# Optimization experiments

Hardware: AMD Instinct MI355X
Metric: run time of the kernel (lower is better)

## Reference

```python
import jax, jax.numpy as jnp
import numpy as np

B, S, D, H = 2, 2048, 512, 8
E = D // H  # per-head depth = 64


def setup_inputs() -> dict:
    key = jax.random.key(0)
    ks = jax.random.split(key, 10)
    x = jax.random.normal(ks[0], (B, S, D), dtype=jnp.float32)
    # binary mask: 1 = masked position (added as -1e9)
    attention_mask = jax.random.randint(ks[1], (B, S, S), 0, 2, dtype=jnp.int32)
    # per-head Dense weights stacked: [H, D, E] (Keras Dense: y = x @ W + b)
    sc = 1.0 / np.sqrt(D)
    Wq = jax.random.normal(ks[2], (H, D, E), dtype=jnp.float32) * sc
    Wk = jax.random.normal(ks[3], (H, D, E), dtype=jnp.float32) * sc
    Wv = jax.random.normal(ks[4], (H, D, E), dtype=jnp.float32) * sc
    bq = jnp.zeros((H, E), dtype=jnp.float32)
    bk = jnp.zeros((H, E), dtype=jnp.float32)
    bv = jnp.zeros((H, E), dtype=jnp.float32)
    Wo = jax.random.normal(ks[5], (D, D), dtype=jnp.float32) * sc
    bo = jnp.zeros((D,), dtype=jnp.float32)
    return {"x": x, "attention_mask": attention_mask, "Wq": Wq, "bq": bq,
            "Wk": Wk, "bk": bk, "Wv": Wv, "bv": bv, "Wo": Wo, "bo": bo}


def reference(x, attention_mask, Wq, bq, Wk, bk, Wv, bv, Wo, bo):
    # Per-head Dense projections, vectorized over heads: [B,H,S,E]
    q = jnp.einsum('bsd,hde->bhse', x, Wq) + bq[None, :, None, :]
    k = jnp.einsum('bsd,hde->bhse', x, Wk) + bk[None, :, None, :]
    v = jnp.einsum('bsd,hde->bhse', x, Wv) + bv[None, :, None, :]
    # scaled dot-product attention
    scores = jnp.einsum('bhse,bhte->bhst', q, k) / jnp.sqrt(jnp.float32(E))
    scores = scores + (-1e9) * attention_mask.astype(jnp.float32)[:, None, :, :]
    weights = jax.nn.softmax(scores, axis=-1)
    o = jnp.einsum('bhst,bhte->bhse', weights, v)
    # concat heads (head i -> columns [i*E:(i+1)*E]) then output Dense
    o = o.transpose(0, 2, 1, 3).reshape(B, S, D)
    return o @ Wo + bo
```

## Files before the change

### kernel.cpp

```cpp
#include <hip/hip_runtime.h>
#include <hip/hip_bf16.h>

typedef unsigned short u16;
typedef unsigned int u32;
typedef unsigned long long u64;
typedef short s16x8 __attribute__((ext_vector_type(8)));
typedef float f32x4 __attribute__((ext_vector_type(4)));
typedef float f32x16 __attribute__((ext_vector_type(16)));
typedef int i32x4 __attribute__((ext_vector_type(4)));

static __device__ __forceinline__ u16 f2b(float f) {
    union { float f; unsigned u; } x; x.f = f;
    unsigned r = x.u + 0x7fffu + ((x.u >> 16) & 1u);
    return (u16)(r >> 16);
}

static __device__ __forceinline__ u32 pkbf2(float a, float b) {
    union { __hip_bfloat162 h; u32 u; } c;
    c.h = __float22bfloat162_rn(make_float2(a, b));
    return c.u;
}

static __device__ __forceinline__ f32x16 zero16() {
    f32x16 z;
#pragma unroll
    for (int i = 0; i < 16; i++) z[i] = 0.f;
    return z;
}

static __device__ __forceinline__ s16x8 mk8(u32 a, u32 b, u32 c, u32 d) {
    union { u32 u[4]; s16x8 v; } x;
    x.u[0] = a; x.u[1] = b; x.u[2] = c; x.u[3] = d;
    return x.v;
}

static __device__ __forceinline__ u32 sx32(u32 v) {
    return (u32)__shfl_xor((int)v, 32, 64);
}

static __device__ __forceinline__ void gll16(const u16* g, u16* l) {
    __builtin_amdgcn_global_load_lds(
        (const __attribute__((address_space(1))) u32*)g,
        (__attribute__((address_space(3))) u32*)l, 16, 0, 0);
}


__global__ __launch_bounds__(256)
void k_pack_all(const float* __restrict__ x, const int* __restrict__ mask,
                const float* __restrict__ Wq, const float* __restrict__ Wk,
                const float* __restrict__ Wv, const float* __restrict__ Wo,
                const float* __restrict__ bq, const float* __restrict__ bk,
                const float* __restrict__ bv, const float* __restrict__ bo,
                u16* __restrict__ xb, u16* __restrict__ WT, u16* __restrict__ WoT,
                float* __restrict__ bias, u32* __restrict__ mb) {
    int idx = blockIdx.x * 256 + threadIdx.x;
    if (idx < 524288) {
        int i = idx * 4;
        float4 v = *(const float4*)(x + i);
        ushort4 o;
        o.x = f2b(v.x); o.y = f2b(v.y); o.z = f2b(v.z); o.w = f2b(v.w);
        *(ushort4*)(xb + i) = o;
    } else if (idx < 1310720) {
        int t = idx - 524288;
        int z = t >> 18, r = t & 262143;
        const float* W = (z == 0) ? Wq : (z == 1) ? Wk : Wv;
        int n = r >> 9, d = r & 511;
        WT[t] = f2b(W[((n >> 6) * 512 + d) * 64 + (n & 63)]);
    } else if (idx < 1572864) {
        int r = idx - 1310720;
        int n = r >> 9, d = r & 511;
        WoT[r] = f2b(Wo[d * 512 + n]);
    } else if (idx < 1574912) {
        int i = idx - 1572864;
        float v;
        if (i < 512) v = bq[i];
        else if (i < 1024) v = bk[i - 512];
        else if (i < 1536) v = bv[i - 1024];
        else v = bo[i - 1536];
        bias[i] = v;
    } else {
        int i2 = idx - 1574912;
        const int* p = mask + (size_t)i2 * 32;
        unsigned wv2 = 0;
#pragma unroll
        for (int j = 0; j < 32; j += 4) {
            int4 v = *(const int4*)(p + j);
            wv2 |= ((unsigned)(v.x & 1) << j) | ((unsigned)(v.y & 1) << (j + 1)) |
                   ((unsigned)(v.z & 1) << (j + 2)) | ((unsigned)(v.w & 1) << (j + 3));
        }
        mb[i2] = wv2;
    }
}


template<int MF, bool F32OUT>
__global__ __launch_bounds__(256)
void k_gemm(const u16* __restrict__ A, const u16* __restrict__ BTbase,
            const float* __restrict__ biasBase,
            u16* __restrict__ Cb, u16* __restrict__ Vt, float* __restrict__ Cf) {
    const int BM = MF * 32;
    const int nblk = blockIdx.x, mblk = blockIdx.y, z = blockIdx.z;
    const u16* BT = BTbase + (size_t)z * 262144;
    const float* bias = biasBase + z * 512;
    __shared__ __align__(16) u16 As[MF * 32 * 64];
    __shared__ __align__(16) u16 Bs[128 * 64];
    const int tid = threadIdx.x, lane = tid & 63, wv = tid >> 6;
    const int lr = lane & 15, lg = lane >> 4;
    const int wr = (wv >> 1) * (MF * 16), wc = (wv & 1) * 64;
    const u16* Ag = A + (size_t)(mblk * BM) * 512;
    const u16* Bg = BT + (size_t)(nblk * 128) * 512;

    f32x4 acc[MF][4];
#pragma unroll
    for (int i = 0; i < MF; i++)
#pragma unroll
        for (int j = 0; j < 4; j++) acc[i][j] = (f32x4){0.f, 0.f, 0.f, 0.f};

    for (int kt = 0; kt < 8; kt++) {
        __syncthreads();
#pragma unroll
        for (int i = 0; i < MF; i++) {
            int f = i * 256 + tid, r = f >> 3, c = f & 7;
            *(i32x4*)&As[r * 64 + ((c * 8) ^ ((r & 7) << 3))] =
                *(const i32x4*)(Ag + (size_t)r * 512 + kt * 64 + c * 8);
        }
#pragma unroll
        for (int i = 0; i < 4; i++) {
            int f = i * 256 + tid, r = f >> 3, c = f & 7;
            *(i32x4*)&Bs[r * 64 + ((c * 8) ^ ((r & 7) << 3))] =
                *(const i32x4*)(Bg + (size_t)r * 512 + kt * 64 + c * 8);
        }
        __syncthreads();
#pragma unroll
        for (int ks = 0; ks < 2; ks++) {
            s16x8 af[MF], bf[4];
#pragma unroll
            for (int mf = 0; mf < MF; mf++) {
                int r = wr + mf * 16 + lr;
                af[mf] = *(const s16x8*)&As[r * 64 + ((ks * 32 + lg * 8) ^ ((r & 7) << 3))];
            }
#pragma unroll
            for (int nf = 0; nf < 4; nf++) {
                int r = wc + nf * 16 + lr;
                bf[nf] = *(const s16x8*)&Bs[r * 64 + ((ks * 32 + lg * 8) ^ ((r & 7) << 3))];
            }
#pragma unroll
            for (int mf = 0; mf < MF; mf++)
#pragma unroll
                for (int nf = 0; nf < 4; nf++)
                    acc[mf][nf] = __builtin_amdgcn_mfma_f32_16x16x32_bf16(
                        af[mf], bf[nf], acc[mf][nf], 0, 0, 0);
        }
    }
    const float qsc = (!F32OUT && z == 0) ? 0.18033688011112042f : 1.0f;
#pragma unroll
    for (int nf = 0; nf < 4; nf++) {
        int col = nblk * 128 + wc + nf * 16 + lr;
        float bval = bias[col];
#pragma unroll
        for (int mf = 0; mf < MF; mf++) {
            int row0 = mblk * BM + wr + mf * 16 + lg * 4;
            if (F32OUT) {
#pragma unroll
                for (int r = 0; r < 4; r++)
                    Cf[(size_t)(row0 + r) * 512 + col] = acc[mf][nf][r] + bval;
            } else if (z == 2) {
                ushort4 o;
                o.x = f2b(acc[mf][nf][0] + bval);
                o.y = f2b(acc[mf][nf][1] + bval);
                o.z = f2b(acc[mf][nf][2] + bval);
                o.w = f2b(acc[mf][nf][3] + bval);
                *(ushort4*)(Vt + (size_t)(row0 >> 11) * 1048576 +
                            (size_t)col * 2048 + (row0 & 2047)) = o;
            } else {
#pragma unroll
                for (int r = 0; r < 4; r++)
                    Cb[(size_t)z * 2097152 + (size_t)(row0 + r) * 512 + col] =
                        f2b((acc[mf][nf][r] + bval) * qsc);
            }
        }
    }
}


__global__ __launch_bounds__(512, 4)
void k_attn(const u16* __restrict__ qkv, const u16* __restrict__ vt,
            const u32* __restrict__ mb, u16* __restrict__ oc) {
    const int qt = blockIdx.x, h = blockIdx.y, b = blockIdx.z;
    const u16* Qb = qkv + (size_t)b * 1048576 + h * 64;
    const u16* Kb = Qb + 2097152;
    const u16* VtH = vt + (size_t)b * 1048576 + (size_t)h * 131072;

    __shared__ __align__(16) u16 SMEM[32768];
    __shared__ float Lbuf[8][32];

    const int tid = threadIdx.x;
    const int lane = tid & 63, w = tid >> 6;
    const int hi = lane >> 5, l31 = lane & 31;
    const int qg = w & 1, kvq = w >> 1;
    const int qrow = qt * 64 + qg * 32 + l31;

    const int lr8 = lane >> 3, lc8 = (lane & 7) ^ lr8;
    const int vr16 = lane >> 2, vc4 = (lane & 3) ^ ((lane >> 3) & 3);
    const int kvbase0 = kvq * 512;
    const int qoff = kvq * 4096;

    s16x8 qf[4];
#pragma unroll
    for (int ks = 0; ks < 4; ks++)
        qf[ks] = *(const s16x8*)(Qb + (size_t)qrow * 512 + ks * 16 + hi * 8);

#pragma unroll
    for (int i = 0; i < 2; i++) {
        gll16(Kb + (size_t)(kvbase0 + qg * 16 + i * 8 + lr8) * 512 + lc8 * 8,
              &SMEM[qoff + (qg * 16 + i * 8) * 64]);
        gll16(VtH + (size_t)(qg * 32 + i * 16 + vr16) * 2048 + kvbase0 + vc4 * 8,
              &SMEM[qoff + 2048 + qg * 1024 + i * 512]);
    }
    const int mbase = (b * 2048 + qrow) * 64 + kvq * 16;
    u32 mreg = mb[mbase];
    __syncthreads();

    f32x16 accO0 = zero16(), accO1 = zero16();
    f32x4 lvec = (f32x4){0.f, 0.f, 0.f, 0.f};
    const int kswz = (l31 & 7) << 3;
    const int vkey = (l31 >> 1) & 3;

    for (int t = 0; t < 16; t++) {
        const int bo = (t & 1) << 14;
        u32 mnx = 0;
        if (t < 15) {
            const int bn = bo ^ 16384;
            const int kvb = kvbase0 + (t + 1) * 32;
#pragma unroll
            for (int i = 0; i < 2; i++) {
                gll16(Kb + (size_t)(kvb + qg * 16 + i * 8 + lr8) * 512 + lc8 * 8,
                      &SMEM[bn + qoff + (qg * 16 + i * 8) * 64]);
                gll16(VtH + (size_t)(qg * 32 + i * 16 + vr16) * 2048 + kvb + vc4 * 8,
                      &SMEM[bn + qoff + 2048 + qg * 1024 + i * 512]);
            }
            mnx = mb[mbase + t + 1];
        }
        const u16* Kq = &SMEM[bo + qoff];
        const u16* Vq = &SMEM[bo + qoff + 2048];

        f32x16 sa = zero16();
        __builtin_amdgcn_s_setprio(1);
#pragma unroll
        for (int ks = 0; ks < 4; ks++) {
            const int cb = ks * 16 + hi * 8;
            s16x8 kf = *(const s16x8*)&Kq[l31 * 64 + (cb ^ kswz)];
            sa = __builtin_amdgcn_mfma_f32_32x32x16_bf16(kf, qf[ks], sa, 0, 0, 0);
        }
        __builtin_amdgcn_s_setprio(0);

        const u32 mw = mreg >> (hi * 4);
        u32 pk[8];
#pragma unroll
        for (int g = 0; g < 8; g++) {
            const int r0 = 2 * g, r1 = 2 * g + 1;
            const int p0 = (r0 & 3) + 8 * (r0 >> 2);
            const int p1 = (r1 & 3) + 8 * (r1 >> 2);
            float a = ((mw >> p0) & 1u) ? 0.f : __builtin_amdgcn_exp2f(sa[r0]);
            float b2 = ((mw >> p1) & 1u) ? 0.f : __builtin_amdgcn_exp2f(sa[r1]);
            lvec[r0 & 3] += a;
            lvec[r1 & 3] += b2;
            pk[g] = pkbf2(a, b2);
        }

        s16x8 pa[2];
        {
            u32 x0 = sx32(pk[0]), x1 = sx32(pk[1]), x2 = sx32(pk[2]), x3 = sx32(pk[3]);
            u32 x4 = sx32(pk[4]), x5 = sx32(pk[5]), x6 = sx32(pk[6]), x7 = sx32(pk[7]);
            pa[0] = mk8(hi ? x2 : pk[0], hi ? x3 : pk[1],
                        hi ? pk[2] : x0, hi ? pk[3] : x1);
            pa[1] = mk8(hi ? x6 : pk[4], hi ? x7 : pk[5],
                        hi ? pk[6] : x4, hi ? pk[7] : x5);
        }

        __builtin_amdgcn_s_setprio(1);
#pragma unroll
        for (int ksg = 0; ksg < 2; ksg++) {
            const int off = ((ksg * 2 + hi) ^ vkey) << 3;
            s16x8 bv0 = *(const s16x8*)&Vq[l31 * 32 + off];
            s16x8 bv1 = *(const s16x8*)&Vq[(32 + l31) * 32 + off];
            accO0 = __builtin_amdgcn_mfma_f32_32x32x16_bf16(pa[ksg], bv0, accO0, 0, 0, 0);
            accO1 = __builtin_amdgcn_mfma_f32_32x32x16_bf16(pa[ksg], bv1, accO1, 0, 0, 0);
        }
        __builtin_amdgcn_s_setprio(0);

        __syncthreads();
        mreg = mnx;
    }

    float Ls = (lvec[0] + lvec[1]) + (lvec[2] + lvec[3]);
    Ls += __shfl_xor(Ls, 32, 64);

    float* Obuf = (float*)SMEM;
    const int lx = (lane & 7) * 4;
    const int obase = w * 2048 + lane * 32;
#pragma unroll
    for (int g = 0; g < 4; g++) {
        *(f32x4*)&Obuf[obase + ((4 * g) ^ lx)] =
            (f32x4){accO0[4 * g], accO0[4 * g + 1], accO0[4 * g + 2], accO0[4 * g + 3]};
        *(f32x4*)&Obuf[obase + ((16 + 4 * g) ^ lx)] =
            (f32x4){accO1[4 * g], accO1[4 * g + 1], accO1[4 * g + 2], accO1[4 * g + 3]};
    }
    if (lane < 32) Lbuf[w][lane] = Ls;
    __syncthreads();

    const int qg2 = w & 1, rq = w >> 1;
    f32x4 v0[4], v1[4];
#pragma unroll
    for (int j = 0; j < 4; j++) {
        const int wp = qg2 + 2 * j;
        v0[j] = *(const f32x4*)&Obuf[wp * 2048 + lane * 32 + ((rq * 4) ^ lx)];
        v1[j] = *(const f32x4*)&Obuf[wp * 2048 + lane * 32 + ((16 + rq * 4) ^ lx)];
    }
#pragma unroll
    for (int k = 0; k < 4; k++) {
        const int q_k = k + 8 * rq + 4 * hi;
        float D = Lbuf[qg2][q_k] + Lbuf[qg2 + 2][q_k] +
                  Lbuf[qg2 + 4][q_k] + Lbuf[qg2 + 6][q_k];
        float inv = 1.0f / D;
        float o0 = (v0[0][k] + v0[1][k] + v0[2][k] + v0[3][k]) * inv;
        float o1 = (v1[0][k] + v1[1][k] + v1[2][k] + v1[3][k]) * inv;
        const size_t orow = ((size_t)b * 2048 + qt * 64 + qg2 * 32 + q_k) * 512 + h * 64;
        oc[orow + l31]      = f2b(o0);
        oc[orow + 32 + l31] = f2b(o1);
    }
}


extern "C" void kernel_launch(void* const* d_in, const int* in_sizes, int n_in,
                              void* d_out, int out_size, void* d_ws, size_t ws_size,
                              hipStream_t stream) {
    const float* x    = (const float*)d_in[0];
    const int*   mask = (const int*)d_in[1];
    const float* Wq   = (const float*)d_in[2];
    const float* bq   = (const float*)d_in[3];
    const float* Wk   = (const float*)d_in[4];
    const float* bk   = (const float*)d_in[5];
    const float* Wv   = (const float*)d_in[6];
    const float* bv   = (const float*)d_in[7];
    const float* Wo   = (const float*)d_in[8];
    const float* bo   = (const float*)d_in[9];

    u16* xb     = (u16*)d_ws;
    u16* WT     = xb + 2097152;
    u16* WoT    = WT + 786432;
    u16* qkv    = WoT + 262144;
    u16* vtp    = qkv + 4194304;
    u16* oc     = qkv + 6291456;
    float* bias = (float*)(oc + 2097152);
    u32* mbits  = (u32*)(bias + 2048);

    k_pack_all<<<7176, 256, 0, stream>>>(x, mask, Wq, Wk, Wv, Wo, bq, bk, bv, bo,
                                         xb, WT, WoT, bias, mbits);
    k_gemm<2, false><<<dim3(4, 64, 3), 256, 0, stream>>>(xb, WT, bias, qkv, vtp, nullptr);
    k_attn<<<dim3(32, 8, 2), 512, 0, stream>>>(qkv, vtp, mbits, oc);
    k_gemm<2, true><<<dim3(4, 64, 1), 256, 0, stream>>>(oc, WoT, bias + 1536,
                                                        nullptr, nullptr, (float*)d_out);
}
```

Measured before the change: 78.80 us.

## Replace mask bits with bf16 AND masks and compute row sums via MFMA

```diff
diff --git a/kernel.cpp b/kernel.cpp
--- a/kernel.cpp
+++ b/kernel.cpp
@@ -52,7 +52,7 @@
                 const float* __restrict__ bq, const float* __restrict__ bk,
                 const float* __restrict__ bv, const float* __restrict__ bo,
                 u16* __restrict__ xb, u16* __restrict__ WT, u16* __restrict__ WoT,
-                float* __restrict__ bias, u32* __restrict__ mb) {
+                float* __restrict__ bias, u32* __restrict__ mand) {
     int idx = blockIdx.x * 256 + threadIdx.x;
     if (idx < 524288) {
         int i = idx * 4;
@@ -80,15 +80,18 @@
         bias[i] = v;
     } else {
         int i2 = idx - 1574912;
-        const int* p = mask + (size_t)i2 * 32;
-        unsigned wv2 = 0;
-#pragma unroll
-        for (int j = 0; j < 32; j += 4) {
-            int4 v = *(const int4*)(p + j);
-            wv2 |= ((unsigned)(v.x & 1) << j) | ((unsigned)(v.y & 1) << (j + 1)) |
-                   ((unsigned)(v.z & 1) << (j + 2)) | ((unsigned)(v.w & 1) << (j + 3));
-        }
-        mb[i2] = wv2;
+        const int4* p = (const int4*)(mask + (size_t)i2 * 32);
+        u32* op = mand + (size_t)i2 * 16;
+#pragma unroll
+        for (int k = 0; k < 4; k++) {
+            int4 v0 = p[2 * k], v1 = p[2 * k + 1];
+            uint4 o;
+            o.x = (v0.x ? 0u : 0xFFFFu) | (v0.y ? 0u : 0xFFFF0000u);
+            o.y = (v0.z ? 0u : 0xFFFFu) | (v0.w ? 0u : 0xFFFF0000u);
+            o.z = (v1.x ? 0u : 0xFFFFu) | (v1.y ? 0u : 0xFFFF0000u);
+            o.w = (v1.z ? 0u : 0xFFFFu) | (v1.w ? 0u : 0xFFFF0000u);
+            *(uint4*)(op + 4 * k) = o;
+        }
     }
 }
 
@@ -185,7 +188,7 @@
 
 __global__ __launch_bounds__(512, 4)
 void k_attn(const u16* __restrict__ qkv, const u16* __restrict__ vt,
-            const u32* __restrict__ mb, u16* __restrict__ oc) {
+            const u32* __restrict__ mand, u16* __restrict__ oc) {
     const int qt = blockIdx.x, h = blockIdx.y, b = blockIdx.z;
     const u16* Qb = qkv + (size_t)b * 1048576 + h * 64;
     const u16* Kb = Qb + 2097152;
@@ -210,36 +213,40 @@
     for (int ks = 0; ks < 4; ks++)
         qf[ks] = *(const s16x8*)(Qb + (size_t)qrow * 512 + ks * 16 + hi * 8);
 
-#pragma unroll
-    for (int i = 0; i < 2; i++) {
-        gll16(Kb + (size_t)(kvbase0 + qg * 16 + i * 8 + lr8) * 512 + lc8 * 8,
-              &SMEM[qoff + (qg * 16 + i * 8) * 64]);
-        gll16(VtH + (size_t)(qg * 32 + i * 16 + vr16) * 2048 + kvbase0 + vc4 * 8,
-              &SMEM[qoff + 2048 + qg * 1024 + i * 512]);
-    }
-    const int mbase = (b * 2048 + qrow) * 64 + kvq * 16;
-    u32 mreg = mb[mbase];
+    const u16* kptr = Kb + (size_t)(kvbase0 + qg * 16 + lr8) * 512 + lc8 * 8;
+    const u16* vptr = VtH + (size_t)(qg * 32 + vr16) * 2048 + kvbase0 + vc4 * 8;
+    const u32* mptr = mand + (size_t)(b * 2048 + qrow) * 1024 + kvq * 256 + 2 * hi;
+
+    gll16(kptr, &SMEM[qoff + (qg * 16) * 64]);
+    gll16(kptr + 4096, &SMEM[qoff + (qg * 16 + 8) * 64]);
+    gll16(vptr, &SMEM[qoff + 2048 + qg * 1024]);
+    gll16(vptr + 32768, &SMEM[qoff + 2048 + qg * 1024 + 512]);
+    uint2 mm0 = *(const uint2*)(mptr);
+    uint2 mm1 = *(const uint2*)(mptr + 4);
+    uint2 mm2 = *(const uint2*)(mptr + 8);
+    uint2 mm3 = *(const uint2*)(mptr + 12);
+    kptr += 16384; vptr += 32; mptr += 16;
     __syncthreads();
 
-    f32x16 accO0 = zero16(), accO1 = zero16();
-    f32x4 lvec = (f32x4){0.f, 0.f, 0.f, 0.f};
+    f32x16 accO0 = zero16(), accO1 = zero16(), lacc = zero16();
+    const s16x8 onesv = mk8(0x3F803F80u, 0x3F803F80u, 0x3F803F80u, 0x3F803F80u);
     const int kswz = (l31 & 7) << 3;
     const int vkey = (l31 >> 1) & 3;
 
     for (int t = 0; t < 16; t++) {
         const int bo = (t & 1) << 14;
-        u32 mnx = 0;
+        uint2 mn0, mn1, mn2, mn3;
         if (t < 15) {
             const int bn = bo ^ 16384;
-            const int kvb = kvbase0 + (t + 1) * 32;
-#pragma unroll
-            for (int i = 0; i < 2; i++) {
-                gll16(Kb + (size_t)(kvb + qg * 16 + i * 8 + lr8) * 512 + lc8 * 8,
-                      &SMEM[bn + qoff + (qg * 16 + i * 8) * 64]);
-                gll16(VtH + (size_t)(qg * 32 + i * 16 + vr16) * 2048 + kvb + vc4 * 8,
-                      &SMEM[bn + qoff + 2048 + qg * 1024 + i * 512]);
-            }
-            mnx = mb[mbase + t + 1];
+            gll16(kptr, &SMEM[bn + qoff + (qg * 16) * 64]);
+            gll16(kptr + 4096, &SMEM[bn + qoff + (qg * 16 + 8) * 64]);
+            gll16(vptr, &SMEM[bn + qoff + 2048 + qg * 1024]);
+            gll16(vptr + 32768, &SMEM[bn + qoff + 2048 + qg * 1024 + 512]);
+            mn0 = *(const uint2*)(mptr);
+            mn1 = *(const uint2*)(mptr + 4);
+            mn2 = *(const uint2*)(mptr + 8);
+            mn3 = *(const uint2*)(mptr + 12);
+            kptr += 16384; vptr += 32; mptr += 16;
         }
         const u16* Kq = &SMEM[bo + qoff];
         const u16* Vq = &SMEM[bo + qoff + 2048];
@@ -254,19 +261,17 @@
         }
         __builtin_amdgcn_s_setprio(0);
 
-        const u32 mw = mreg >> (hi * 4);
         u32 pk[8];
 #pragma unroll
         for (int g = 0; g < 8; g++) {
-            const int r0 = 2 * g, r1 = 2 * g + 1;
-            const int p0 = (r0 & 3) + 8 * (r0 >> 2);
-            const int p1 = (r1 & 3) + 8 * (r1 >> 2);
-            float a = ((mw >> p0) & 1u) ? 0.f : __builtin_amdgcn_exp2f(sa[r0]);
-            float b2 = ((mw >> p1) & 1u) ? 0.f : __builtin_amdgcn_exp2f(sa[r1]);
-            lvec[r0 & 3] += a;
-            lvec[r1 & 3] += b2;
+            float a = __builtin_amdgcn_exp2f(sa[2 * g]);
+            float b2 = __builtin_amdgcn_exp2f(sa[2 * g + 1]);
             pk[g] = pkbf2(a, b2);
         }
+        pk[0] &= mm0.x; pk[1] &= mm0.y;
+        pk[2] &= mm1.x; pk[3] &= mm1.y;
+        pk[4] &= mm2.x; pk[5] &= mm2.y;
+        pk[6] &= mm3.x; pk[7] &= mm3.y;
 
         s16x8 pa[2];
         {
@@ -287,18 +292,24 @@
             accO0 = __builtin_amdgcn_mfma_f32_32x32x16_bf16(pa[ksg], bv0, accO0, 0, 0, 0);
             accO1 = __builtin_amdgcn_mfma_f32_32x32x16_bf16(pa[ksg], bv1, accO1, 0, 0, 0);
         }
+        lacc = __builtin_amdgcn_mfma_f32_32x32x16_bf16(pa[0], onesv, lacc, 0, 0, 0);
+        lacc = __builtin_amdgcn_mfma_f32_32x32x16_bf16(pa[1], onesv, lacc, 0, 0, 0);
         __builtin_amdgcn_s_setprio(0);
 
         __syncthreads();
-        mreg = mnx;
-    }
-
-    float Ls = (lvec[0] + lvec[1]) + (lvec[2] + lvec[3]);
-    Ls += __shfl_xor(Ls, 32, 64);
+        if (t < 15) { mm0 = mn0; mm1 = mn1; mm2 = mn2; mm3 = mn3; }
+    }
+
+    if (l31 == 0) {
+#pragma unroll
+        for (int r = 0; r < 16; r++)
+            Lbuf[w][(r & 3) + 8 * (r >> 2) + 4 * hi] = lacc[r];
+    }
 
     float* Obuf = (float*)SMEM;
     const int lx = (lane & 7) * 4;
     const int obase = w * 2048 + lane * 32;
+    __syncthreads();
 #pragma unroll
     for (int g = 0; g < 4; g++) {
         *(f32x4*)&Obuf[obase + ((4 * g) ^ lx)] =
@@ -306,7 +317,6 @@
         *(f32x4*)&Obuf[obase + ((16 + 4 * g) ^ lx)] =
             (f32x4){accO1[4 * g], accO1[4 * g + 1], accO1[4 * g + 2], accO1[4 * g + 3]};
     }
-    if (lane < 32) Lbuf[w][lane] = Ls;
     __syncthreads();
 
     const int qg2 = w & 1, rq = w >> 1;
@@ -353,12 +363,12 @@
     u16* vtp    = qkv + 4194304;
     u16* oc     = qkv + 6291456;
     float* bias = (float*)(oc + 2097152);
-    u32* mbits  = (u32*)(bias + 2048);
+    u32* mand   = (u32*)(bias + 2048);
 
     k_pack_all<<<7176, 256, 0, stream>>>(x, mask, Wq, Wk, Wv, Wo, bq, bk, bv, bo,
-                                         xb, WT, WoT, bias, mbits);
+                                         xb, WT, WoT, bias, mand);
     k_gemm<2, false><<<dim3(4, 64, 3), 256, 0, stream>>>(xb, WT, bias, qkv, vtp, nullptr);
-    k_attn<<<dim3(32, 8, 2), 512, 0, stream>>>(qkv, vtp, mbits, oc);
+    k_attn<<<dim3(32, 8, 2), 512, 0, stream>>>(qkv, vtp, mand, oc);
     k_gemm<2, true><<<dim3(4, 64, 1), 256, 0, stream>>>(oc, WoT, bias + 1536,
                                                         nullptr, nullptr, (float*)d_out);
 }
```

After: 101.7 us. +29.0%, slower.

## Restructure attention to 4 waves each owning KV quarter for 64 query rows

Applied to the files above, without the earlier changes.

```diff
diff --git a/kernel.cpp b/kernel.cpp
--- a/kernel.cpp
+++ b/kernel.cpp
@@ -183,7 +183,7 @@
 }
 
 
-__global__ __launch_bounds__(512, 4)
+__global__ __launch_bounds__(256, 2)
 void k_attn(const u16* __restrict__ qkv, const u16* __restrict__ vt,
             const u32* __restrict__ mb, u16* __restrict__ oc) {
     const int qt = blockIdx.x, h = blockIdx.y, b = blockIdx.z;
@@ -192,90 +192,112 @@
     const u16* VtH = vt + (size_t)b * 1048576 + (size_t)h * 131072;
 
     __shared__ __align__(16) u16 SMEM[32768];
-    __shared__ float Lbuf[8][32];
+    __shared__ float Lbuf[4][64];
 
     const int tid = threadIdx.x;
     const int lane = tid & 63, w = tid >> 6;
     const int hi = lane >> 5, l31 = lane & 31;
-    const int qg = w & 1, kvq = w >> 1;
-    const int qrow = qt * 64 + qg * 32 + l31;
+    const int qrow = qt * 64 + l31;
+
+    s16x8 qfl[4], qfh[4];
+#pragma unroll
+    for (int ks = 0; ks < 4; ks++) {
+        qfl[ks] = *(const s16x8*)(Qb + (size_t)qrow * 512 + ks * 16 + hi * 8);
+        qfh[ks] = *(const s16x8*)(Qb + (size_t)(qrow + 32) * 512 + ks * 16 + hi * 8);
+    }
 
     const int lr8 = lane >> 3, lc8 = (lane & 7) ^ lr8;
     const int vr16 = lane >> 2, vc4 = (lane & 3) ^ ((lane >> 3) & 3);
-    const int kvbase0 = kvq * 512;
-    const int qoff = kvq * 4096;
-
-    s16x8 qf[4];
-#pragma unroll
-    for (int ks = 0; ks < 4; ks++)
-        qf[ks] = *(const s16x8*)(Qb + (size_t)qrow * 512 + ks * 16 + hi * 8);
-
-#pragma unroll
-    for (int i = 0; i < 2; i++) {
-        gll16(Kb + (size_t)(kvbase0 + qg * 16 + i * 8 + lr8) * 512 + lc8 * 8,
-              &SMEM[qoff + (qg * 16 + i * 8) * 64]);
-        gll16(VtH + (size_t)(qg * 32 + i * 16 + vr16) * 2048 + kvbase0 + vc4 * 8,
-              &SMEM[qoff + 2048 + qg * 1024 + i * 512]);
-    }
-    const int mbase = (b * 2048 + qrow) * 64 + kvq * 16;
-    u32 mreg = mb[mbase];
-    __syncthreads();
-
-    f32x16 accO0 = zero16(), accO1 = zero16();
-    f32x4 lvec = (f32x4){0.f, 0.f, 0.f, 0.f};
+    const int kv0 = w * 512;
+
+    const u16* kptr = Kb + (size_t)(kv0 + lr8) * 512 + lc8 * 8;
+    const u16* vptr = VtH + (size_t)vr16 * 2048 + kv0 + vc4 * 8;
+    const u32* mbl = mb + (size_t)(b * 2048 + qrow) * 64 + w * 16;
+    const u32* mbh = mbl + 2048;
+
+    u16* wbase = &SMEM[w * 8192];
+
+#pragma unroll
+    for (int i = 0; i < 4; i++) {
+        gll16(kptr + (size_t)(i * 8) * 512, wbase + i * 512);
+        gll16(vptr + (size_t)(i * 16) * 2048, wbase + 2048 + i * 512);
+    }
+    u32 ml = mbl[0], mh = mbh[0];
+
+    f32x16 aL0 = zero16(), aL1 = zero16(), aH0 = zero16(), aH1 = zero16();
+    f32x4 lvl = (f32x4){0.f, 0.f, 0.f, 0.f}, lvh = (f32x4){0.f, 0.f, 0.f, 0.f};
     const int kswz = (l31 & 7) << 3;
     const int vkey = (l31 >> 1) & 3;
 
     for (int t = 0; t < 16; t++) {
-        const int bo = (t & 1) << 14;
-        u32 mnx = 0;
+        const u16* Kq = wbase + (t & 1) * 4096;
+        const u16* Vq = Kq + 2048;
+        u32 mnl = 0, mnh = 0;
         if (t < 15) {
-            const int bn = bo ^ 16384;
-            const int kvb = kvbase0 + (t + 1) * 32;
-#pragma unroll
-            for (int i = 0; i < 2; i++) {
-                gll16(Kb + (size_t)(kvb + qg * 16 + i * 8 + lr8) * 512 + lc8 * 8,
-                      &SMEM[bn + qoff + (qg * 16 + i * 8) * 64]);
-                gll16(VtH + (size_t)(qg * 32 + i * 16 + vr16) * 2048 + kvb + vc4 * 8,
-                      &SMEM[bn + qoff + 2048 + qg * 1024 + i * 512]);
-            }
-            mnx = mb[mbase + t + 1];
-        }
-        const u16* Kq = &SMEM[bo + qoff];
-        const u16* Vq = &SMEM[bo + qoff + 2048];
-
-        f32x16 sa = zero16();
+            const u16* kp = kptr + (size_t)((t + 1) * 32) * 512;
+            const u16* vp = vptr + (t + 1) * 32;
+            u16* db = wbase + (((t + 1) & 1) << 12);
+#pragma unroll
+            for (int i = 0; i < 4; i++) {
+                gll16(kp + (size_t)(i * 8) * 512, db + i * 512);
+                gll16(vp + (size_t)(i * 16) * 2048, db + 2048 + i * 512);
+            }
+            mnl = mbl[t + 1];
+            mnh = mbh[t + 1];
+            asm volatile("s_waitcnt vmcnt(10)" ::: "memory");
+        } else {
+            asm volatile("s_waitcnt vmcnt(0)" ::: "memory");
+        }
+        __builtin_amdgcn_sched_barrier(0);
+
+        f32x16 sl = zero16(), sh = zero16();
         __builtin_amdgcn_s_setprio(1);
 #pragma unroll
         for (int ks = 0; ks < 4; ks++) {
-            const int cb = ks * 16 + hi * 8;
-            s16x8 kf = *(const s16x8*)&Kq[l31 * 64 + (cb ^ kswz)];
-            sa = __builtin_amdgcn_mfma_f32_32x32x16_bf16(kf, qf[ks], sa, 0, 0, 0);
+            s16x8 kf = *(const s16x8*)&Kq[l31 * 64 + ((ks * 16 + hi * 8) ^ kswz)];
+            sl = __builtin_amdgcn_mfma_f32_32x32x16_bf16(kf, qfl[ks], sl, 0, 0, 0);
+            sh = __builtin_amdgcn_mfma_f32_32x32x16_bf16(kf, qfh[ks], sh, 0, 0, 0);
         }
         __builtin_amdgcn_s_setprio(0);
 
-        const u32 mw = mreg >> (hi * 4);
-        u32 pk[8];
-#pragma unroll
-        for (int g = 0; g < 8; g++) {
-            const int r0 = 2 * g, r1 = 2 * g + 1;
-            const int p0 = (r0 & 3) + 8 * (r0 >> 2);
-            const int p1 = (r1 & 3) + 8 * (r1 >> 2);
-            float a = ((mw >> p0) & 1u) ? 0.f : __builtin_amdgcn_exp2f(sa[r0]);
-            float b2 = ((mw >> p1) & 1u) ? 0.f : __builtin_amdgcn_exp2f(sa[r1]);
-            lvec[r0 & 3] += a;
-            lvec[r1 & 3] += b2;
-            pk[g] = pkbf2(a, b2);
-        }
-
-        s16x8 pa[2];
+        s16x8 pal0, pal1, pah0, pah1;
         {
-            u32 x0 = sx32(pk[0]), x1 = sx32(pk[1]), x2 = sx32(pk[2]), x3 = sx32(pk[3]);
-            u32 x4 = sx32(pk[4]), x5 = sx32(pk[5]), x6 = sx32(pk[6]), x7 = sx32(pk[7]);
-            pa[0] = mk8(hi ? x2 : pk[0], hi ? x3 : pk[1],
-                        hi ? pk[2] : x0, hi ? pk[3] : x1);
-            pa[1] = mk8(hi ? x6 : pk[4], hi ? x7 : pk[5],
-                        hi ? pk[6] : x4, hi ? pk[7] : x5);
+            const u32 mw = ml >> (hi * 4);
+            u32 pk[8];
+#pragma unroll
+            for (int g = 0; g < 8; g++) {
+                const int p0 = ((2 * g) & 3) + 8 * (g >> 1);
+                float a = ((mw >> p0) & 1u) ? 0.f : __builtin_amdgcn_exp2f(sl[2 * g]);
+                float b2 = ((mw >> (p0 + 1)) & 1u) ? 0.f : __builtin_amdgcn_exp2f(sl[2 * g + 1]);
+                lvl[(2 * g) & 3] += a;
+                lvl[(2 * g + 1) & 3] += b2;
+                pk[g] = pkbf2(a, b2);
+            }
+            u32 xa = sx32(hi ? pk[0] : pk[2]);
+            u32 xb = sx32(hi ? pk[1] : pk[3]);
+            u32 xc = sx32(hi ? pk[4] : pk[6]);
+            u32 xd = sx32(hi ? pk[5] : pk[7]);
+            pal0 = hi ? mk8(xa, xb, pk[2], pk[3]) : mk8(pk[0], pk[1], xa, xb);
+            pal1 = hi ? mk8(xc, xd, pk[6], pk[7]) : mk8(pk[4], pk[5], xc, xd);
+        }
+        {
+            const u32 mw = mh >> (hi * 4);
+            u32 pk[8];
+#pragma unroll
+            for (int g = 0; g < 8; g++) {
+                const int p0 = ((2 * g) & 3) + 8 * (g >> 1);
+                float a = ((mw >> p0) & 1u) ? 0.f : __builtin_amdgcn_exp2f(sh[2 * g]);
+                float b2 = ((mw >> (p0 + 1)) & 1u) ? 0.f : __builtin_amdgcn_exp2f(sh[2 * g + 1]);
+                lvh[(2 * g) & 3] += a;
+                lvh[(2 * g + 1) & 3] += b2;
+                pk[g] = pkbf2(a, b2);
+            }
+            u32 xa = sx32(hi ? pk[0] : pk[2]);
+            u32 xb = sx32(hi ? pk[1] : pk[3]);
+            u32 xc = sx32(hi ? pk[4] : pk[6]);
+            u32 xd = sx32(hi ? pk[5] : pk[7]);
+            pah0 = hi ? mk8(xa, xb, pk[2], pk[3]) : mk8(pk[0], pk[1], xa, xb);
+            pah1 = hi ? mk8(xc, xd, pk[6], pk[7]) : mk8(pk[4], pk[5], xc, xd);
         }
 
         __builtin_amdgcn_s_setprio(1);
@@ -284,50 +306,59 @@
             const int off = ((ksg * 2 + hi) ^ vkey) << 3;
             s16x8 bv0 = *(const s16x8*)&Vq[l31 * 32 + off];
             s16x8 bv1 = *(const s16x8*)&Vq[(32 + l31) * 32 + off];
-            accO0 = __builtin_amdgcn_mfma_f32_32x32x16_bf16(pa[ksg], bv0, accO0, 0, 0, 0);
-            accO1 = __builtin_amdgcn_mfma_f32_32x32x16_bf16(pa[ksg], bv1, accO1, 0, 0, 0);
+            s16x8 pl = ksg ? pal1 : pal0;
+            s16x8 ph = ksg ? pah1 : pah0;
+            aL0 = __builtin_amdgcn_mfma_f32_32x32x16_bf16(pl, bv0, aL0, 0, 0, 0);
+            aL1 = __builtin_amdgcn_mfma_f32_32x32x16_bf16(pl, bv1, aL1, 0, 0, 0);
+            aH0 = __builtin_amdgcn_mfma_f32_32x32x16_bf16(ph, bv0, aH0, 0, 0, 0);
+            aH1 = __builtin_amdgcn_mfma_f32_32x32x16_bf16(ph, bv1, aH1, 0, 0, 0);
         }
         __builtin_amdgcn_s_setprio(0);
 
-        __syncthreads();
-        mreg = mnx;
-    }
-
-    float Ls = (lvec[0] + lvec[1]) + (lvec[2] + lvec[3]);
-    Ls += __shfl_xor(Ls, 32, 64);
+        ml = mnl; mh = mnh;
+    }
+
+    float Lsl = (lvl[0] + lvl[1]) + (lvl[2] + lvl[3]);
+    Lsl += __shfl_xor(Lsl, 32, 64);
+    float Lsh = (lvh[0] + lvh[1]) + (lvh[2] + lvh[3]);
+    Lsh += __shfl_xor(Lsh, 32, 64);
+    if (lane < 32) { Lbuf[w][l31] = Lsl; Lbuf[w][32 + l31] = Lsh; }
 
     float* Obuf = (float*)SMEM;
     const int lx = (lane & 7) * 4;
-    const int obase = w * 2048 + lane * 32;
+    const int ob = w * 4096 + lane * 32;
 #pragma unroll
     for (int g = 0; g < 4; g++) {
-        *(f32x4*)&Obuf[obase + ((4 * g) ^ lx)] =
-            (f32x4){accO0[4 * g], accO0[4 * g + 1], accO0[4 * g + 2], accO0[4 * g + 3]};
-        *(f32x4*)&Obuf[obase + ((16 + 4 * g) ^ lx)] =
-            (f32x4){accO1[4 * g], accO1[4 * g + 1], accO1[4 * g + 2], accO1[4 * g + 3]};
-    }
-    if (lane < 32) Lbuf[w][lane] = Ls;
+        *(f32x4*)&Obuf[ob + ((4 * g) ^ lx)] =
+            (f32x4){aL0[4 * g], aL0[4 * g + 1], aL0[4 * g + 2], aL0[4 * g + 3]};
+        *(f32x4*)&Obuf[ob + ((16 + 4 * g) ^ lx)] =
+            (f32x4){aL1[4 * g], aL1[4 * g + 1], aL1[4 * g + 2], aL1[4 * g + 3]};
+        *(f32x4*)&Obuf[ob + 2048 + ((4 * g) ^ lx)] =
+            (f32x4){aH0[4 * g], aH0[4 * g + 1], aH0[4 * g + 2], aH0[4 * g + 3]};
+        *(f32x4*)&Obuf[ob + 2048 + ((16 + 4 * g) ^ lx)] =
+            (f32x4){aH1[4 * g], aH1[4 * g + 1], aH1[4 * g + 2], aH1[4 * g + 3]};
+    }
     __syncthreads();
 
-    const int qg2 = w & 1, rq = w >> 1;
-    f32x4 v0[4], v1[4];
-#pragma unroll
-    for (int j = 0; j < 4; j++) {
-        const int wp = qg2 + 2 * j;
-        v0[j] = *(const f32x4*)&Obuf[wp * 2048 + lane * 32 + ((rq * 4) ^ lx)];
-        v1[j] = *(const f32x4*)&Obuf[wp * 2048 + lane * 32 + ((16 + rq * 4) ^ lx)];
-    }
-#pragma unroll
-    for (int k = 0; k < 4; k++) {
-        const int q_k = k + 8 * rq + 4 * hi;
-        float D = Lbuf[qg2][q_k] + Lbuf[qg2 + 2][q_k] +
-                  Lbuf[qg2 + 4][q_k] + Lbuf[qg2 + 6][q_k];
-        float inv = 1.0f / D;
-        float o0 = (v0[0][k] + v0[1][k] + v0[2][k] + v0[3][k]) * inv;
-        float o1 = (v1[0][k] + v1[1][k] + v1[2][k] + v1[3][k]) * inv;
-        const size_t orow = ((size_t)b * 2048 + qt * 64 + qg2 * 32 + q_k) * 512 + h * 64;
-        oc[orow + l31]      = f2b(o0);
-        oc[orow + 32 + l31] = f2b(o1);
+    const int qg2 = w & 1, eh = w >> 1;
+    const int rb2 = qg2 * 2048 + lane * 32;
+#pragma unroll
+    for (int g = 0; g < 4; g++) {
+        const int off = (16 * eh + 4 * g) ^ lx;
+        f32x4 s0 = *(const f32x4*)&Obuf[rb2 + off];
+        f32x4 s1 = *(const f32x4*)&Obuf[4096 + rb2 + off];
+        f32x4 s2 = *(const f32x4*)&Obuf[8192 + rb2 + off];
+        f32x4 s3 = *(const f32x4*)&Obuf[12288 + rb2 + off];
+        f32x4 sum = (s0 + s1) + (s2 + s3);
+#pragma unroll
+        for (int j = 0; j < 4; j++) {
+            const int q = j + 4 * hi + 8 * g;
+            float D = Lbuf[0][qg2 * 32 + q] + Lbuf[1][qg2 * 32 + q] +
+                      Lbuf[2][qg2 * 32 + q] + Lbuf[3][qg2 * 32 + q];
+            const size_t orow = ((size_t)b * 2048 + qt * 64 + qg2 * 32 + q) * 512 +
+                                h * 64 + eh * 32;
+            oc[orow + l31] = f2b(sum[j] / D);
+        }
     }
 }
 
@@ -358,7 +389,7 @@
     k_pack_all<<<7176, 256, 0, stream>>>(x, mask, Wq, Wk, Wv, Wo, bq, bk, bv, bo,
                                          xb, WT, WoT, bias, mbits);
     k_gemm<2, false><<<dim3(4, 64, 3), 256, 0, stream>>>(xb, WT, bias, qkv, vtp, nullptr);
-    k_attn<<<dim3(32, 8, 2), 512, 0, stream>>>(qkv, vtp, mbits, oc);
+    k_attn<<<dim3(32, 8, 2), 256, 0, stream>>>(qkv, vtp, mbits, oc);
     k_gemm<2, true><<<dim3(4, 64, 1), 256, 0, stream>>>(oc, WoT, bias + 1536,
                                                         nullptr, nullptr, (float*)d_out);
 }
```

Measured after the change: 80.04 us. Within noise of the previous version (+1.6%).
